# Optimization experiments

Measured on AMD Instinct MI355X. Metric: run time of the kernel, lower is better.

Reference implementation:

```python
import jax, jax.numpy as jnp
import numpy as np

B, T, Z, S, H = 32, 128, 100, 6, 64
F1, F2 = 512, 128


def setup_inputs() -> dict:
    key = jax.random.key(0)
    ks = jax.random.split(key, 11)
    g = lambda k, shape, sc: (jax.random.normal(k, shape, dtype=jnp.float32) * sc)
    return {
        "x": jax.random.normal(ks[0], (B, T, Z, S), dtype=jnp.float32),
        "W_ih": g(ks[1], (3 * H, S), 0.125),   # GRU input weights [r|z|n]
        "W_hh": g(ks[2], (3 * H, H), 0.125),   # GRU hidden weights [r|z|n]
        "b_ih": g(ks[3], (3 * H,), 0.125),
        "b_hh": g(ks[4], (3 * H,), 0.125),
        "w1": g(ks[5], (F1, H), 0.1),
        "b1": g(ks[6], (F1,), 0.1),
        "w2": g(ks[7], (F2, F1), 0.04),
        "b2": g(ks[8], (F2,), 0.04),
        "w3": g(ks[9], (1, F2), 0.09),
        "b3": g(ks[10], (1,), 0.09),
    }


def reference(x, W_ih, W_hh, b_ih, b_hh, w1, b1, w2, b2, w3, b3):
    b, t, z, s = x.shape
    h_dim = W_hh.shape[1]
    # Fuse the per-zone python loop into the batch dim, zone-major so the
    # final reshape matches torch.stack(a).view(-1, t, nzones).
    xm = jnp.transpose(x, (2, 0, 1, 3)).reshape(z * b, t, s)  # (ZB, T, S)
    # Precompute input projections for all timesteps (one big GEMM).
    gi_all = jnp.einsum('nts,gs->ntg', xm, W_ih) + b_ih        # (ZB, T, 3H)

    def step(h, gi):
        gh = h @ W_hh.T + b_hh
        r = jax.nn.sigmoid(gi[:, :h_dim] + gh[:, :h_dim])
        zg = jax.nn.sigmoid(gi[:, h_dim:2 * h_dim] + gh[:, h_dim:2 * h_dim])
        n = jnp.tanh(gi[:, 2 * h_dim:] + r * gh[:, 2 * h_dim:])
        h_new = (1.0 - zg) * n + zg * h
        return h_new, h_new

    h0 = jnp.zeros((z * b, h_dim), x.dtype)
    _, sx = jax.lax.scan(step, h0, jnp.swapaxes(gi_all, 0, 1))  # (T, ZB, H)
    sx = jnp.swapaxes(sx, 0, 1)                                  # (ZB, T, H)

    a1 = jax.nn.relu(sx @ w1.T + b1)
    a2 = jax.nn.relu(a1 @ w2.T + b2)
    a3 = a2 @ w3.T + b3                                          # (ZB, T, 1)
    return a3.reshape(-1, t, z)                                  # (B, T, Z)
```

## Files before the change

kernel.cpp:

```cpp
#include <hip/hip_runtime.h>
#include <stdint.h>

#define Tdim 128
#define Zdim 100
#define Sdim 6
#define Hdim 64
#define ZB   3200
#define F1   512
#define F2   128
#define Mrows (ZB * Tdim)

typedef _Float16 f16x8 __attribute__((ext_vector_type(8)));
typedef _Float16 f16x4 __attribute__((ext_vector_type(4)));
typedef float f32x4 __attribute__((ext_vector_type(4)));
typedef uint32_t u32x4 __attribute__((ext_vector_type(4)));

__device__ __forceinline__ float fast_rcp(float x) {
  return __builtin_amdgcn_rcpf(x);
}

__global__ __launch_bounds__(256) void prep_kernel(
    const float* __restrict__ W_ih, const float* __restrict__ W_hh,
    const float* __restrict__ w1, const float* __restrict__ w2,
    _Float16* __restrict__ Wf, _Float16* __restrict__ w1p,
    _Float16* __restrict__ w2p) {
  int i = blockIdx.x * 256 + threadIdx.x;
  if (i < 192 * 96) {
    int g = i / 96, k = i - g * 96;
    float v = (k < 64) ? W_hh[g * 64 + k] : ((k < 70) ? W_ih[g * 6 + (k - 64)] : 0.f);
    Wf[i] = (_Float16)v;
  }
  int j = i - 192 * 96;
  if (j >= 0 && j < 32768) {
    int kt = j >> 11, ntl = (j >> 10) & 1, kf = (j >> 9) & 1;
    int lane = (j >> 3) & 63, e = j & 7;
    int q = lane >> 4, c = lane & 15;
    int row = kt * 32 + ntl * 16 + c;
    int h = kf * 32 + q * 8 + e;
    w1p[j] = (_Float16)w1[row * 64 + h];
  }
  int l = j - 32768;
  if (l >= 0 && l < 65536) {
    int kt = l >> 12, nt = (l >> 9) & 7;
    int lane = (l >> 3) & 63, e = l & 7;
    int q = lane >> 4, c = lane & 15;
    int row = nt * 16 + c;
    int k = kt * 32 + q * 8 + e;
    w2p[l] = (_Float16)w2[row * 512 + k];
  }
}

__global__ __launch_bounds__(512, 1) void gru_kernel(
    const float* __restrict__ x, const _Float16* __restrict__ Wf,
    const float* __restrict__ b_ih, const float* __restrict__ b_hh,
    _Float16* __restrict__ sx) {
  __shared__ __align__(16) _Float16 hist[16][32][72];
  __shared__ __align__(16) _Float16 xs[Tdim][32][8];
  const int tid = threadIdx.x;
  const int lane = tid & 63;
  const int w8 = tid >> 6;
  const int s = w8 >> 2;
  const int w = w8 & 3;
  const int c = lane & 15;
  const int q = lane >> 4;
  const int s16c = s * 16 + c;

  for (int i = 0; i < 8; i++) {
    int idx = i * 512 + tid;
    int t = idx >> 5, row = idx & 31;
    int nr = blockIdx.x * 32 + row;
    const float* p = x + (size_t)(nr & 31) * (Tdim * Zdim * Sdim)
                       + (size_t)t * (Zdim * Sdim) + (size_t)(nr >> 5) * Sdim;
    f16x8 v;
    v[0] = (_Float16)p[0]; v[1] = (_Float16)p[1]; v[2] = (_Float16)p[2];
    v[3] = (_Float16)p[3]; v[4] = (_Float16)p[4]; v[5] = (_Float16)p[5];
    v[6] = (_Float16)0.f;  v[7] = (_Float16)0.f;
    *(f16x8*)&xs[t][row][0] = v;
  }

  const int gr0 = w * 16;
  const int gz0 = 64 + w * 16;
  const int gn0 = 128 + w * 16;

  f16x8 Ar[3], Az[3], Anh[2], Ani;
#pragma unroll
  for (int kf = 0; kf < 3; kf++) {
    Ar[kf] = *(const f16x8*)(Wf + (size_t)(gr0 + c) * 96 + kf * 32 + q * 8);
    Az[kf] = *(const f16x8*)(Wf + (size_t)(gz0 + c) * 96 + kf * 32 + q * 8);
  }
  Anh[0] = *(const f16x8*)(Wf + (size_t)(gn0 + c) * 96 + q * 8);
  Anh[1] = *(const f16x8*)(Wf + (size_t)(gn0 + c) * 96 + 32 + q * 8);
  Ani    = *(const f16x8*)(Wf + (size_t)(gn0 + c) * 96 + 64 + q * 8);

  f32x4 Cr, Cz, Cnh, Cni;
  {
    f32x4 bir = *(const f32x4*)(b_ih + gr0 + q * 4);
    f32x4 bhr = *(const f32x4*)(b_hh + gr0 + q * 4);
    f32x4 biz = *(const f32x4*)(b_ih + gz0 + q * 4);
    f32x4 bhz = *(const f32x4*)(b_hh + gz0 + q * 4);
#pragma unroll
    for (int r = 0; r < 4; r++) { Cr[r] = bir[r] + bhr[r]; Cz[r] = biz[r] + bhz[r]; }
    Cnh = *(const f32x4*)(b_hh + gn0 + q * 4);
    Cni = *(const f32x4*)(b_ih + gn0 + q * 4);
  }

  const uint32_t xmask = (q == 0) ? 0xffffffffu : 0u;

  __syncthreads();

  f16x8 Bh0 = {0, 0, 0, 0, 0, 0, 0, 0};
  f16x8 Bh1 = {0, 0, 0, 0, 0, 0, 0, 0};
  f32x4 hprev = {0.f, 0.f, 0.f, 0.f};

  f32x4 Dr_s, Dz_s, Dni_s;
  {
    u32x4 xv = *(const u32x4*)&xs[0][s16c][0];
    xv[0] &= xmask; xv[1] &= xmask; xv[2] &= xmask; xv[3] &= xmask;
    f16x8 Bx = *(f16x8*)&xv;
    Dni_s = __builtin_amdgcn_mfma_f32_16x16x32_f16(Ani, Bx, Cni, 0, 0, 0);
    Dr_s  = __builtin_amdgcn_mfma_f32_16x16x32_f16(Ar[2], Bx, Cr, 0, 0, 0);
    Dz_s  = __builtin_amdgcn_mfma_f32_16x16x32_f16(Az[2], Bx, Cz, 0, 0, 0);
  }

#pragma unroll 1
  for (int tch = 0; tch < 8; tch++) {
#pragma unroll 1
    for (int tc = 0; tc < 16; tc++) {
      const int t = tch * 16 + tc;
      f32x4 Dnh = __builtin_amdgcn_mfma_f32_16x16x32_f16(Anh[0], Bh0, Cnh, 0, 0, 0);
      f32x4 Dr  = __builtin_amdgcn_mfma_f32_16x16x32_f16(Ar[0], Bh0, Dr_s, 0, 0, 0);
      f32x4 Dz  = __builtin_amdgcn_mfma_f32_16x16x32_f16(Az[0], Bh0, Dz_s, 0, 0, 0);
      Dnh = __builtin_amdgcn_mfma_f32_16x16x32_f16(Anh[1], Bh1, Dnh, 0, 0, 0);
      Dr  = __builtin_amdgcn_mfma_f32_16x16x32_f16(Ar[1], Bh1, Dr, 0, 0, 0);
      Dz  = __builtin_amdgcn_mfma_f32_16x16x32_f16(Az[1], Bh1, Dz, 0, 0, 0);

      f16x4 pk;
#pragma unroll
      for (int r = 0; r < 4; r++) {
        float er = __expf(-Dr[r]);
        float rr = fast_rcp(1.f + er);
        float ez = __expf(-Dz[r]);
        float zg = fast_rcp(1.f + ez);
        float na = Dni_s[r] + rr * Dnh[r];
        float en = __expf(2.f * na);
        float nn = 1.f - 2.f * fast_rcp(en + 1.f);
        float hnew = nn + zg * (hprev[r] - nn);
        hprev[r] = hnew;
        pk[r] = (_Float16)hnew;
      }
      *(f16x4*)&hist[tc][s16c][w * 16 + q * 4] = pk;

      if (t + 1 < Tdim) {
        u32x4 xv = *(const u32x4*)&xs[t + 1][s16c][0];
        xv[0] &= xmask; xv[1] &= xmask; xv[2] &= xmask; xv[3] &= xmask;
        f16x8 Bx = *(f16x8*)&xv;
        Dni_s = __builtin_amdgcn_mfma_f32_16x16x32_f16(Ani, Bx, Cni, 0, 0, 0);
        Dr_s  = __builtin_amdgcn_mfma_f32_16x16x32_f16(Ar[2], Bx, Cr, 0, 0, 0);
        Dz_s  = __builtin_amdgcn_mfma_f32_16x16x32_f16(Az[2], Bx, Cz, 0, 0, 0);
      }
      __syncthreads();
      Bh0 = *(const f16x8*)&hist[tc][s16c][q * 8];
      Bh1 = *(const f16x8*)&hist[tc][s16c][32 + q * 8];
    }
    {
      const int t0 = tch * 16;
#pragma unroll
      for (int rr2 = 0; rr2 < 4; rr2++) {
        const int row = w8 * 4 + rr2;
        const int nrow = blockIdx.x * 32 + row;
        _Float16* dst = sx + (size_t)nrow * Tdim * Hdim + (size_t)t0 * Hdim;
#pragma unroll
        for (int it = 0; it < 2; it++) {
          int idx = it * 64 + lane;
          int tcc = idx >> 3, hd8 = idx & 7;
          f16x8 vv = *(const f16x8*)&hist[tcc][row][hd8 * 8];
          *(f16x8*)(dst + tcc * 64 + hd8 * 8) = vv;
        }
      }
      __syncthreads();
    }
  }
}

__global__ __launch_bounds__(256, 2) void mlp_kernel(
    const _Float16* __restrict__ sx, const _Float16* __restrict__ w1p,
    const _Float16* __restrict__ w2p, const float* __restrict__ b1,
    const float* __restrict__ b2, const float* __restrict__ w3,
    const float* __restrict__ b3, float* __restrict__ out) {
  __shared__ __align__(16) _Float16 w1s[32768];
  __shared__ __align__(16) _Float16 rep[4][4][512];
  const int tid = threadIdx.x;
  const int lane = tid & 63;
  const int wave = tid >> 6;
  const int c = lane & 15;
  const int q = lane >> 4;
  const size_t m0 = ((size_t)blockIdx.x * 4 + wave) * 64;

  {
    const u32x4* src = (const u32x4*)w1p;
    u32x4* dst = (u32x4*)w1s;
#pragma unroll
    for (int i = 0; i < 16; i++)
      dst[i * 256 + tid] = src[i * 256 + tid];
  }

  f16x8 Bs[4][2];
#pragma unroll
  for (int g = 0; g < 4; g++)
#pragma unroll
    for (int kk = 0; kk < 2; kk++)
      Bs[g][kk] = *(const f16x8*)(sx + (m0 + g * 16 + c) * Hdim + kk * 32 + q * 8);

  f32x4 acc2[4][8];
#pragma unroll
  for (int g = 0; g < 4; g++)
#pragma unroll
    for (int nt = 0; nt < 8; nt++) acc2[g][nt] = (f32x4){0.f, 0.f, 0.f, 0.f};

  __syncthreads();

  {
#pragma unroll
    for (int ntl = 0; ntl < 2; ntl++) {
      f16x8 A0 = *(const f16x8*)&w1s[ntl * 1024 + lane * 8];
      f16x8 A1 = *(const f16x8*)&w1s[ntl * 1024 + 512 + lane * 8];
      f32x4 bb = *(const f32x4*)(b1 + ntl * 16 + q * 4);
      const int roff = ((2 * ntl + (q >> 1)) * 16 + c) * 8 + (q & 1) * 4;
#pragma unroll
      for (int g = 0; g < 4; g++) {
        f32x4 cc = __builtin_amdgcn_mfma_f32_16x16x32_f16(A0, Bs[g][0], bb, 0, 0, 0);
        cc = __builtin_amdgcn_mfma_f32_16x16x32_f16(A1, Bs[g][1], cc, 0, 0, 0);
        f16x4 pk;
#pragma unroll
        for (int r = 0; r < 4; r++)
          pk[r] = (_Float16)(cc[r] > 0.f ? cc[r] : 0.f);
        *(f16x4*)&rep[wave][g][roff] = pk;
      }
    }
  }

#pragma unroll 1
  for (int kt = 0; kt < 16; kt++) {
    const int ktn = kt + 1;
    const bool more = (ktn < 16);
    f16x8 A2[8];
#pragma unroll
    for (int nt = 0; nt < 8; nt++)
      A2[nt] = *(const f16x8*)(w2p + (size_t)kt * 4096 + nt * 512 + lane * 8);
    f16x8 W0[2], W1[2];
    f32x4 bb[2];
    {
      const int kts = more ? ktn : kt;
#pragma unroll
      for (int ntl = 0; ntl < 2; ntl++) {
        W0[ntl] = *(const f16x8*)&w1s[kts * 2048 + ntl * 1024 + lane * 8];
        W1[ntl] = *(const f16x8*)&w1s[kts * 2048 + ntl * 1024 + 512 + lane * 8];
        bb[ntl] = *(const f32x4*)(b1 + kts * 32 + ntl * 16 + q * 4);
      }
    }
    f16x8 Ba[4];
#pragma unroll
    for (int g = 0; g < 4; g++)
      Ba[g] = *(const f16x8*)&rep[wave][g][lane * 8];

    if (more) {
#pragma unroll
      for (int ntl = 0; ntl < 2; ntl++) {
        const int roff = ((2 * ntl + (q >> 1)) * 16 + c) * 8 + (q & 1) * 4;
#pragma unroll
        for (int g = 0; g < 4; g++) {
          f32x4 cc = __builtin_amdgcn_mfma_f32_16x16x32_f16(W0[ntl], Bs[g][0], bb[ntl], 0, 0, 0);
          cc = __builtin_amdgcn_mfma_f32_16x16x32_f16(W1[ntl], Bs[g][1], cc, 0, 0, 0);
          f16x4 pk;
#pragma unroll
          for (int r = 0; r < 4; r++)
            pk[r] = (_Float16)(cc[r] > 0.f ? cc[r] : 0.f);
          *(f16x4*)&rep[wave][g][roff] = pk;
        }
      }
    }

#pragma unroll
    for (int nt = 0; nt < 8; nt++)
#pragma unroll
      for (int g = 0; g < 4; g++)
        acc2[g][nt] = __builtin_amdgcn_mfma_f32_16x16x32_f16(A2[nt], Ba[g], acc2[g][nt], 0, 0, 0);
  }

  float part[4] = {0.f, 0.f, 0.f, 0.f};
#pragma unroll
  for (int nt = 0; nt < 8; nt++) {
    f32x4 bb = *(const f32x4*)(b2 + nt * 16 + q * 4);
    f32x4 ww = *(const f32x4*)(w3 + nt * 16 + q * 4);
#pragma unroll
    for (int g = 0; g < 4; g++) {
#pragma unroll
      for (int r = 0; r < 4; r++) {
        float v = acc2[g][nt][r] + bb[r];
        v = v > 0.f ? v : 0.f;
        part[g] = fmaf(v, ww[r], part[g]);
      }
    }
  }
#pragma unroll
  for (int g = 0; g < 4; g++) {
    part[g] += __shfl_xor(part[g], 16, 64);
    part[g] += __shfl_xor(part[g], 32, 64);
  }
  float pv = (q == 0) ? part[0] : (q == 1) ? part[1] : (q == 2) ? part[2] : part[3];
  out[m0 + q * 16 + c] = pv + b3[0];
}

extern "C" void kernel_launch(void* const* d_in, const int* in_sizes, int n_in,
                              void* d_out, int out_size, void* d_ws, size_t ws_size,
                              hipStream_t stream) {
  const float* x    = (const float*)d_in[0];
  const float* W_ih = (const float*)d_in[1];
  const float* W_hh = (const float*)d_in[2];
  const float* b_ih = (const float*)d_in[3];
  const float* b_hh = (const float*)d_in[4];
  const float* w1   = (const float*)d_in[5];
  const float* b1   = (const float*)d_in[6];
  const float* w2   = (const float*)d_in[7];
  const float* b2   = (const float*)d_in[8];
  const float* w3   = (const float*)d_in[9];
  const float* b3   = (const float*)d_in[10];
  float* out = (float*)d_out;

  char* ws = (char*)d_ws;
  _Float16* sxf = (_Float16*)ws;
  _Float16* Wf  = (_Float16*)(ws + 52428800);
  _Float16* w1p = (_Float16*)(ws + 52428800 + 36864);
  _Float16* w2p = (_Float16*)(ws + 52428800 + 36864 + 65536);

  hipLaunchKernelGGL(prep_kernel, dim3(456), dim3(256), 0, stream,
                     W_ih, W_hh, w1, w2, Wf, w1p, w2p);
  hipLaunchKernelGGL(gru_kernel, dim3(ZB / 32), dim3(512), 0, stream,
                     x, Wf, b_ih, b_hh, sxf);
  hipLaunchKernelGGL(mlp_kernel, dim3(Mrows / 256), dim3(256), 0, stream,
                     sxf, w1p, w2p, b1, b2, w3, b3, out);
}
```

Measured before the change: 239.8 us.

## Halve GRU block size so each wave handles both 16-row column groups

The GRU kernel drops from 512 to 256 threads per block. Each wave now processes two 16-row column groups (cg loop) instead of one, interleaving independent MFMA chains across the groups. This gives each wave more instruction-level parallelism, makes each per-step barrier cover fewer waves, and allows two blocks per CU. The cost is higher register pressure per wave, and only 100 blocks are launched, so overall occupancy stays low.

```diff
diff --git a/kernel.cpp b/kernel.cpp
--- a/kernel.cpp
+++ b/kernel.cpp
@@ -50,7 +50,7 @@
   }
 }
 
-__global__ __launch_bounds__(512, 1) void gru_kernel(
+__global__ __launch_bounds__(256, 2) void gru_kernel(
     const float* __restrict__ x, const _Float16* __restrict__ Wf,
     const float* __restrict__ b_ih, const float* __restrict__ b_hh,
     _Float16* __restrict__ sx) {
@@ -58,15 +58,12 @@
   __shared__ __align__(16) _Float16 xs[Tdim][32][8];
   const int tid = threadIdx.x;
   const int lane = tid & 63;
-  const int w8 = tid >> 6;
-  const int s = w8 >> 2;
-  const int w = w8 & 3;
+  const int w = tid >> 6;
   const int c = lane & 15;
   const int q = lane >> 4;
-  const int s16c = s * 16 + c;
-
-  for (int i = 0; i < 8; i++) {
-    int idx = i * 512 + tid;
+
+  for (int i = 0; i < 16; i++) {
+    int idx = i * 256 + tid;
     int t = idx >> 5, row = idx & 31;
     int nr = blockIdx.x * 32 + row;
     const float* p = x + (size_t)(nr & 31) * (Tdim * Zdim * Sdim)
@@ -108,18 +105,24 @@
 
   __syncthreads();
 
-  f16x8 Bh0 = {0, 0, 0, 0, 0, 0, 0, 0};
-  f16x8 Bh1 = {0, 0, 0, 0, 0, 0, 0, 0};
-  f32x4 hprev = {0.f, 0.f, 0.f, 0.f};
-
-  f32x4 Dr_s, Dz_s, Dni_s;
-  {
-    u32x4 xv = *(const u32x4*)&xs[0][s16c][0];
+  f16x8 Bh0[2], Bh1[2];
+  f32x4 hprev[2];
+#pragma unroll
+  for (int cg = 0; cg < 2; cg++) {
+    Bh0[cg] = (f16x8){0, 0, 0, 0, 0, 0, 0, 0};
+    Bh1[cg] = (f16x8){0, 0, 0, 0, 0, 0, 0, 0};
+    hprev[cg] = (f32x4){0.f, 0.f, 0.f, 0.f};
+  }
+
+  f32x4 Sr[2], Sz[2], Sni[2];
+#pragma unroll
+  for (int cg = 0; cg < 2; cg++) {
+    u32x4 xv = *(const u32x4*)&xs[0][cg * 16 + c][0];
     xv[0] &= xmask; xv[1] &= xmask; xv[2] &= xmask; xv[3] &= xmask;
     f16x8 Bx = *(f16x8*)&xv;
-    Dni_s = __builtin_amdgcn_mfma_f32_16x16x32_f16(Ani, Bx, Cni, 0, 0, 0);
-    Dr_s  = __builtin_amdgcn_mfma_f32_16x16x32_f16(Ar[2], Bx, Cr, 0, 0, 0);
-    Dz_s  = __builtin_amdgcn_mfma_f32_16x16x32_f16(Az[2], Bx, Cz, 0, 0, 0);
+    Sni[cg] = __builtin_amdgcn_mfma_f32_16x16x32_f16(Ani, Bx, Cni, 0, 0, 0);
+    Sr[cg]  = __builtin_amdgcn_mfma_f32_16x16x32_f16(Ar[2], Bx, Cr, 0, 0, 0);
+    Sz[cg]  = __builtin_amdgcn_mfma_f32_16x16x32_f16(Az[2], Bx, Cz, 0, 0, 0);
   }
 
 #pragma unroll 1
@@ -127,46 +130,68 @@
 #pragma unroll 1
     for (int tc = 0; tc < 16; tc++) {
       const int t = tch * 16 + tc;
-      f32x4 Dnh = __builtin_amdgcn_mfma_f32_16x16x32_f16(Anh[0], Bh0, Cnh, 0, 0, 0);
-      f32x4 Dr  = __builtin_amdgcn_mfma_f32_16x16x32_f16(Ar[0], Bh0, Dr_s, 0, 0, 0);
-      f32x4 Dz  = __builtin_amdgcn_mfma_f32_16x16x32_f16(Az[0], Bh0, Dz_s, 0, 0, 0);
-      Dnh = __builtin_amdgcn_mfma_f32_16x16x32_f16(Anh[1], Bh1, Dnh, 0, 0, 0);
-      Dr  = __builtin_amdgcn_mfma_f32_16x16x32_f16(Ar[1], Bh1, Dr, 0, 0, 0);
-      Dz  = __builtin_amdgcn_mfma_f32_16x16x32_f16(Az[1], Bh1, Dz, 0, 0, 0);
-
-      f16x4 pk;
-#pragma unroll
-      for (int r = 0; r < 4; r++) {
-        float er = __expf(-Dr[r]);
-        float rr = fast_rcp(1.f + er);
-        float ez = __expf(-Dz[r]);
-        float zg = fast_rcp(1.f + ez);
-        float na = Dni_s[r] + rr * Dnh[r];
-        float en = __expf(2.f * na);
-        float nn = 1.f - 2.f * fast_rcp(en + 1.f);
-        float hnew = nn + zg * (hprev[r] - nn);
-        hprev[r] = hnew;
-        pk[r] = (_Float16)hnew;
-      }
-      *(f16x4*)&hist[tc][s16c][w * 16 + q * 4] = pk;
+      f32x4 Dnh[2], Dr[2], Dz[2];
+#pragma unroll
+      for (int cg = 0; cg < 2; cg++)
+        Dnh[cg] = __builtin_amdgcn_mfma_f32_16x16x32_f16(Anh[0], Bh0[cg], Cnh, 0, 0, 0);
+#pragma unroll
+      for (int cg = 0; cg < 2; cg++)
+        Dr[cg] = __builtin_amdgcn_mfma_f32_16x16x32_f16(Ar[0], Bh0[cg], Sr[cg], 0, 0, 0);
+#pragma unroll
+      for (int cg = 0; cg < 2; cg++)
+        Dz[cg] = __builtin_amdgcn_mfma_f32_16x16x32_f16(Az[0], Bh0[cg], Sz[cg], 0, 0, 0);
+#pragma unroll
+      for (int cg = 0; cg < 2; cg++)
+        Dnh[cg] = __builtin_amdgcn_mfma_f32_16x16x32_f16(Anh[1], Bh1[cg], Dnh[cg], 0, 0, 0);
+#pragma unroll
+      for (int cg = 0; cg < 2; cg++)
+        Dr[cg] = __builtin_amdgcn_mfma_f32_16x16x32_f16(Ar[1], Bh1[cg], Dr[cg], 0, 0, 0);
+#pragma unroll
+      for (int cg = 0; cg < 2; cg++)
+        Dz[cg] = __builtin_amdgcn_mfma_f32_16x16x32_f16(Az[1], Bh1[cg], Dz[cg], 0, 0, 0);
+
+#pragma unroll
+      for (int cg = 0; cg < 2; cg++) {
+        f16x4 pk;
+#pragma unroll
+        for (int r = 0; r < 4; r++) {
+          float er = __expf(-Dr[cg][r]);
+          float rr = fast_rcp(1.f + er);
+          float ez = __expf(-Dz[cg][r]);
+          float zg = fast_rcp(1.f + ez);
+          float na = Sni[cg][r] + rr * Dnh[cg][r];
+          float en = __expf(2.f * na);
+          float nn = 1.f - 2.f * fast_rcp(en + 1.f);
+          float hnew = nn + zg * (hprev[cg][r] - nn);
+          hprev[cg][r] = hnew;
+          pk[r] = (_Float16)hnew;
+        }
+        *(f16x4*)&hist[tc][cg * 16 + c][w * 16 + q * 4] = pk;
+      }
 
       if (t + 1 < Tdim) {
-        u32x4 xv = *(const u32x4*)&xs[t + 1][s16c][0];
-        xv[0] &= xmask; xv[1] &= xmask; xv[2] &= xmask; xv[3] &= xmask;
-        f16x8 Bx = *(f16x8*)&xv;
-        Dni_s = __builtin_amdgcn_mfma_f32_16x16x32_f16(Ani, Bx, Cni, 0, 0, 0);
-        Dr_s  = __builtin_amdgcn_mfma_f32_16x16x32_f16(Ar[2], Bx, Cr, 0, 0, 0);
-        Dz_s  = __builtin_amdgcn_mfma_f32_16x16x32_f16(Az[2], Bx, Cz, 0, 0, 0);
+#pragma unroll
+        for (int cg = 0; cg < 2; cg++) {
+          u32x4 xv = *(const u32x4*)&xs[t + 1][cg * 16 + c][0];
+          xv[0] &= xmask; xv[1] &= xmask; xv[2] &= xmask; xv[3] &= xmask;
+          f16x8 Bx = *(f16x8*)&xv;
+          Sni[cg] = __builtin_amdgcn_mfma_f32_16x16x32_f16(Ani, Bx, Cni, 0, 0, 0);
+          Sr[cg]  = __builtin_amdgcn_mfma_f32_16x16x32_f16(Ar[2], Bx, Cr, 0, 0, 0);
+          Sz[cg]  = __builtin_amdgcn_mfma_f32_16x16x32_f16(Az[2], Bx, Cz, 0, 0, 0);
+        }
       }
       __syncthreads();
-      Bh0 = *(const f16x8*)&hist[tc][s16c][q * 8];
-      Bh1 = *(const f16x8*)&hist[tc][s16c][32 + q * 8];
+#pragma unroll
+      for (int cg = 0; cg < 2; cg++) {
+        Bh0[cg] = *(const f16x8*)&hist[tc][cg * 16 + c][q * 8];
+        Bh1[cg] = *(const f16x8*)&hist[tc][cg * 16 + c][32 + q * 8];
+      }
     }
     {
       const int t0 = tch * 16;
 #pragma unroll
-      for (int rr2 = 0; rr2 < 4; rr2++) {
-        const int row = w8 * 4 + rr2;
+      for (int rr2 = 0; rr2 < 8; rr2++) {
+        const int row = w * 8 + rr2;
         const int nrow = blockIdx.x * 32 + row;
         _Float16* dst = sx + (size_t)nrow * Tdim * Hdim + (size_t)t0 * Hdim;
 #pragma unroll
@@ -335,7 +360,7 @@
 
   hipLaunchKernelGGL(prep_kernel, dim3(456), dim3(256), 0, stream,
                      W_ih, W_hh, w1, w2, Wf, w1p, w2p);
-  hipLaunchKernelGGL(gru_kernel, dim3(ZB / 32), dim3(512), 0, stream,
+  hipLaunchKernelGGL(gru_kernel, dim3(ZB / 32), dim3(256), 0, stream,
                      x, Wf, b_ih, b_hh, sxf);
   hipLaunchKernelGGL(mlp_kernel, dim3(Mrows / 256), dim3(256), 0, stream,
                      sxf, w1p, w2p, b1, b2, w3, b3, out);
```

Result: slower. 257.6 us (+7.4%).
